# Kernel tuning notes

Hardware: AMD Instinct MI355X
Metric: run time of the kernel (lower is better)

## Reference

```python
import jax, jax.numpy as jnp
import numpy as np

DIM, H, KV, HD = 2048, 32, 8, 64
NREP = H // KV
EPS = 1e-6
NEG = -1e30


def _rope(x, cos, sin):
    # x: [B,S,h,HD], cos/sin: [S,HD//2]
    xr, xi = x[..., 0::2], x[..., 1::2]
    c = cos[None, :, None, :]
    s = sin[None, :, None, :]
    out = jnp.stack([xr * c - xi * s, xr * s + xi * c], axis=-1)
    return out.reshape(x.shape)


def _rmsnorm(x, w):
    xf = x.astype(jnp.float32)
    inv = jax.lax.rsqrt(jnp.mean(xf * xf, axis=-1, keepdims=True) + EPS)
    return (xf * inv * w).astype(x.dtype)


def setup_inputs() -> dict:
    key = jax.random.key(0)
    ks = jax.random.split(key, 9)
    B, S = 1, 2048
    x = jax.random.normal(ks[0], (B, S, DIM), jnp.float32)
    cos = jax.random.uniform(ks[1], (S, HD // 2), jnp.float32)
    sin = jax.random.uniform(ks[2], (S, HD // 2), jnp.float32)
    sc = 1.0 / np.sqrt(DIM)
    wq = jax.random.normal(ks[3], (DIM, DIM), jnp.float32) * sc
    wk = jax.random.normal(ks[4], (KV * HD, DIM), jnp.float32) * sc
    wv = jax.random.normal(ks[5], (KV * HD, DIM), jnp.float32) * sc
    wo = jax.random.normal(ks[6], (DIM, DIM), jnp.float32) * sc
    wg = jax.random.normal(ks[7], (DIM, DIM), jnp.float32) * sc
    qn = jnp.ones((HD,), jnp.float32)
    kn = jnp.ones((HD,), jnp.float32)
    return {"x": x, "cos": cos, "sin": sin, "wq": wq, "wk": wk, "wv": wv,
            "wo": wo, "wg": wg, "qn": qn, "kn": kn}


def reference(x, cos, sin, wq, wk, wv, wo, wg, qn, kn):
    B, S, _ = x.shape
    q = (x @ wq.T).reshape(B, S, H, HD)
    k = (x @ wk.T).reshape(B, S, KV, HD)
    v = (x @ wv.T).reshape(B, S, KV, HD)
    q = _rope(q, cos, sin)
    k = _rope(k, cos, sin)
    q = _rmsnorm(q, qn)
    k = _rmsnorm(k, kn)
    # GQA without materializing repeat_kv: head h = g*NREP + r uses kv head g
    qg = q.reshape(B, S, KV, NREP, HD)
    scale = 1.0 / np.sqrt(HD)
    scores = jnp.einsum('bqgrd,bkgd->bgrqk', qg, k) * scale  # [B,KV,NREP,S,S]
    causal = jnp.tril(jnp.ones((S, S), bool))
    scores = jnp.where(causal, scores, NEG)
    attn = jax.nn.softmax(scores, axis=-1)
    o = jnp.einsum('bgrqk,bkgd->bqgrd', attn, v).reshape(B, S, DIM)
    o = o * jax.nn.sigmoid(x @ wg.T)
    return o @ wo.T
```

## Files before the change

kernel.cpp:

```cpp
#include <hip/hip_runtime.h>
#include <stdint.h>

typedef unsigned short u16;
typedef __bf16 bf16x8 __attribute__((ext_vector_type(8)));
typedef float f32x4 __attribute__((ext_vector_type(4)));

__device__ __forceinline__ float bf2f(u16 u) {
  union { unsigned int i; float f; } v; v.i = ((unsigned int)u) << 16; return v.f;
}
__device__ __forceinline__ u16 f2bf(float f) {
  union { float f; unsigned int i; } v; v.f = f;
  unsigned int r = v.i + 0x7fffu + ((v.i >> 16) & 1u);
  return (u16)(r >> 16);
}
__device__ __forceinline__ u16 f2bf_trunc(float f) {
  union { float f; unsigned int i; } v; v.f = f;
  return (u16)(v.i >> 16);
}
__device__ __forceinline__ void ld16(const void* g, void* l) {
  __builtin_amdgcn_global_load_lds(
      (const __attribute__((address_space(1))) unsigned int*)g,
      (__attribute__((address_space(3))) unsigned int*)l, 16, 0, 0);
}

__global__ __launch_bounds__(256) void k_cast(
    const float* __restrict__ s0, u16* __restrict__ d0,
    const float* __restrict__ s1, u16* __restrict__ d1,
    const float* __restrict__ s2, u16* __restrict__ d2,
    const float* __restrict__ s3, u16* __restrict__ d3,
    const float* __restrict__ s4, u16* __restrict__ d4,
    const float* __restrict__ s5, u16* __restrict__ d5)
{
  int b = blockIdx.x;
  const float* s; u16* d;
  if (b < 4096)       { s = s0; d = d0; }
  else if (b < 8192)  { s = s1; d = d1; b -= 4096; }
  else if (b < 9216)  { s = s2; d = d2; b -= 8192; }
  else if (b < 10240) { s = s3; d = d3; b -= 9216; }
  else if (b < 14336) { s = s4; d = d4; b -= 10240; }
  else                { s = s5; d = d5; b -= 14336; }
  const int i = (b * 256 + threadIdx.x) * 4;
  const float4 v = *(const float4*)(s + i);
  ushort4 o;
  o.x = f2bf(v.x); o.y = f2bf(v.y); o.z = f2bf(v.z); o.w = f2bf(v.w);
  *(ushort4*)(d + i) = o;
}

template <typename OT>
__device__ __forceinline__ void gemm_body(
    const u16* __restrict__ A, int lda,
    const u16* __restrict__ B, int ldb,
    OT* __restrict__ C, int ldc, int K,
    u16* As, u16* Bs)
{
  const int tid = threadIdx.x;
  const int wave = tid >> 6, lane = tid & 63;
  const int wrow = (wave >> 1) * 64, wcol = (wave & 1) * 64;
  const int fr = lane & 15, kg = lane >> 4;
  const int srl = lane >> 3;
  const int scg = (lane & 7) ^ srl;

  f32x4 acc[4][4];
  const f32x4 z = {0.f, 0.f, 0.f, 0.f};
  for (int i = 0; i < 4; i++) for (int j = 0; j < 4; j++) acc[i][j] = z;

  const u16* Ag = A + (size_t)(wave * 8 + srl) * lda + scg * 8;
  const u16* Bg = B + (size_t)(wave * 8 + srl) * ldb + scg * 8;
  u16* Asw = As + wave * 8 * 64;
  u16* Bsw = Bs + wave * 8 * 64;
  const int sxr = fr & 7;

  for (int k0 = 0; k0 < K; k0 += 64) {
    for (int i = 0; i < 4; i++) {
      ld16(Ag + k0 + (size_t)(i * 32) * lda, Asw + i * 32 * 64);
      ld16(Bg + k0 + (size_t)(i * 32) * ldb, Bsw + i * 32 * 64);
    }
    __syncthreads();
    bf16x8 af[4][2], bfr[4][2];
    for (int i = 0; i < 4; i++)
      for (int h = 0; h < 2; h++) {
        af[i][h]  = *(const bf16x8*)&As[(wrow + i * 16 + fr) * 64 + (((h * 4 + kg) ^ sxr)) * 8];
        bfr[i][h] = *(const bf16x8*)&Bs[(wcol + i * 16 + fr) * 64 + (((h * 4 + kg) ^ sxr)) * 8];
      }
    for (int h = 0; h < 2; h++)
      for (int mi = 0; mi < 4; mi++)
        for (int ni = 0; ni < 4; ni++)
          acc[mi][ni] = __builtin_amdgcn_mfma_f32_16x16x32_bf16(af[mi][h], bfr[ni][h], acc[mi][ni], 0, 0, 0);
    __syncthreads();
  }
  const int er = kg * 4, ec = fr;
  for (int mi = 0; mi < 4; mi++)
    for (int ni = 0; ni < 4; ni++)
      for (int r = 0; r < 4; r++) {
        const float v = acc[mi][ni][r];
        OT* p = C + (size_t)(wrow + mi * 16 + er + r) * ldc + wcol + ni * 16 + ec;
        if constexpr (sizeof(OT) == 2) *p = (OT)f2bf(v); else *p = (OT)v;
      }
}

__global__ __launch_bounds__(256) void k_gemm_qkvg(
    const u16* __restrict__ x, const u16* __restrict__ wq, const u16* __restrict__ wk,
    const u16* __restrict__ wv, const u16* __restrict__ wg, u16* __restrict__ out)
{
  __shared__ __align__(16) u16 As[128 * 64];
  __shared__ __align__(16) u16 Bs[128 * 64];
  const int m0 = blockIdx.x * 128;
  const int c0 = blockIdx.y * 128;
  const u16* B; int br;
  if (c0 < 2048)      { B = wq; br = c0; }
  else if (c0 < 2560) { B = wk; br = c0 - 2048; }
  else if (c0 < 3072) { B = wv; br = c0 - 2560; }
  else                { B = wg; br = c0 - 3072; }
  gemm_body<u16>(x + (size_t)m0 * 2048, 2048, B + (size_t)br * 2048, 2048,
                 out + (size_t)m0 * 5120 + c0, 5120, 2048, As, Bs);
}

__global__ __launch_bounds__(256) void k_gemm_out(
    const u16* __restrict__ a, const u16* __restrict__ wo, float* __restrict__ out)
{
  __shared__ __align__(16) u16 As[128 * 64];
  __shared__ __align__(16) u16 Bs[128 * 64];
  const int m0 = blockIdx.x * 128;
  const int c0 = blockIdx.y * 128;
  gemm_body<float>(a + (size_t)m0 * 2048, 2048, wo + (size_t)c0 * 2048, 2048,
                   out + (size_t)m0 * 2048 + c0, 2048, 2048, As, Bs);
}

__global__ __launch_bounds__(256) void k_prep(
    u16* __restrict__ qkvg, const float* __restrict__ cosp, const float* __restrict__ sinp,
    const float* __restrict__ qn, const float* __restrict__ kn, u16* __restrict__ vt)
{
  __shared__ u16 Ls[64 * 72];
  if (blockIdx.x < 10240) {
    const int wid = (blockIdx.x * 256 + threadIdx.x) >> 6;
    const int lane = threadIdx.x & 63;
    const int s = wid / 20, hp = wid - s * 20;
    const int h = hp * 2 + (lane >> 5);
    const int j = lane & 31;
    u16* base; const float* wn;
    if (h < 32) { base = qkvg + (size_t)s * 5120 + h * 64;                wn = qn; }
    else        { base = qkvg + (size_t)s * 5120 + 2048 + (h - 32) * 64; wn = kn; }
    const unsigned int u = *(const unsigned int*)(base + 2 * j);
    const float xr = bf2f((u16)(u & 0xffffu)), xi = bf2f((u16)(u >> 16));
    const float c = cosp[s * 32 + j], sn = sinp[s * 32 + j];
    const float o0 = xr * c - xi * sn;
    const float o1 = xr * sn + xi * c;
    float ss = o0 * o0 + o1 * o1;
    for (int m = 1; m <= 16; m <<= 1) ss += __shfl_xor(ss, m, 64);
    const float inv = rsqrtf(ss * (1.0f / 64.0f) + 1e-6f);
    const u16 r0 = f2bf(o0 * inv * wn[2 * j]);
    const u16 r1 = f2bf(o1 * inv * wn[2 * j + 1]);
    *(unsigned int*)(base + 2 * j) = (unsigned int)r0 | ((unsigned int)r1 << 16);
  } else {
    const int bb = blockIdx.x - 10240;
    const int s0 = (bb & 31) * 64, g0 = (bb >> 5) * 64;
    const int tid = threadIdx.x;
    const int lr = tid >> 4, lc = (tid & 15) * 4;
    for (int p = 0; p < 4; p++) {
      const int r = p * 16 + lr;
      *(ushort4*)&Ls[r * 72 + lc] = *(const ushort4*)&qkvg[(size_t)(s0 + r) * 5120 + 2560 + g0 + lc];
    }
    __syncthreads();
    for (int p = 0; p < 4; p++) {
      const int r = p * 16 + lr;
      ushort4 o;
      o.x = Ls[(lc + 0) * 72 + r];
      o.y = Ls[(lc + 1) * 72 + r];
      o.z = Ls[(lc + 2) * 72 + r];
      o.w = Ls[(lc + 3) * 72 + r];
      *(ushort4*)&vt[(size_t)(g0 + r) * 2048 + s0 + lc] = o;
    }
  }
}

__global__ __launch_bounds__(256) void k_attn_part(
    const u16* __restrict__ qkvg, const u16* __restrict__ vt,
    u16* __restrict__ part, float* __restrict__ ml)
{
  __shared__ __align__(16) u16 Ks[128 * 64];
  __shared__ __align__(16) u16 Vs[64 * 128];
  __shared__ __align__(16) u16 Ps[64 * 132];
  const int c = blockIdx.x, h = blockIdx.y, g = h >> 2;
  int qt, ci;
  if (c < 8)       { qt = c;                 ci = 0; }
  else if (c < 24) { qt = 8 + ((c - 8) >> 1);  ci = (c - 8) & 1; }
  else if (c < 48) { qt = 16 + (c - 24) / 3;   ci = (c - 24) % 3; }
  else             { qt = 24 + ((c - 48) >> 2); ci = (c - 48) & 3; }
  const int kb0 = ci * 512;
  const int kend = min(kb0 + 512, (qt + 1) * 64);
  const int q0 = qt * 64;
  const int tid = threadIdx.x, wave = tid >> 6, lane = tid & 63;
  const int fr = lane & 15, kg = lane >> 4, fq = kg * 8;
  const int sx = fr & 7;

  {
    const u16* Qg = qkvg + (size_t)(q0 + wave * 16 + (lane >> 3)) * 5120 + h * 64 + (lane & 7) * 8;
    ld16(Qg, Ks + wave * 1024);
    ld16(Qg + (size_t)8 * 5120, Ks + wave * 1024 + 512);
  }
  __syncthreads();
  const bf16x8 aq0 = *(const bf16x8*)&Ks[(wave * 16 + fr) * 64 + fq];
  const bf16x8 aq1 = *(const bf16x8*)&Ks[(wave * 16 + fr) * 64 + 32 + fq];
  __syncthreads();

  f32x4 o[4];
  const f32x4 z = {0.f, 0.f, 0.f, 0.f};
  for (int i = 0; i < 4; i++) o[i] = z;
  float lsum[4] = {0.f, 0.f, 0.f, 0.f};
  const int qrow = q0 + wave * 16 + kg * 4;

  const int krl = wave * 8 + (lane >> 3);
  const int kcg = (lane & 7) ^ (krl & 7);
  const int vrl = wave * 4 + kg;
  const int vcg = fr ^ (vrl & 7);

  for (int kb = kb0; kb < kend; kb += 128) {
    {
      const u16* Kg = qkvg + (size_t)(kb + krl) * 5120 + 2048 + g * 64 + kcg * 8;
      for (int i = 0; i < 4; i++)
        ld16(Kg + (size_t)(i * 32) * 5120, Ks + (i * 32 + wave * 8) * 64);
    }
    {
      const u16* Vg = vt + (size_t)(g * 64 + vrl) * 2048 + kb + vcg * 8;
      for (int i = 0; i < 4; i++)
        ld16(Vg + (size_t)(i * 16) * 2048, Vs + (i * 16 + wave * 4) * 128);
    }
    __syncthreads();

    f32x4 sc[8];
    for (int i = 0; i < 8; i++) sc[i] = z;
    for (int ni = 0; ni < 8; ni++) {
      const bf16x8 bk0 = *(const bf16x8*)&Ks[(ni * 16 + fr) * 64 + (kg ^ sx) * 8];
      const bf16x8 bk1 = *(const bf16x8*)&Ks[(ni * 16 + fr) * 64 + ((kg + 4) ^ sx) * 8];
      sc[ni] = __builtin_amdgcn_mfma_f32_16x16x32_bf16(aq0, bk0, sc[ni], 0, 0, 0);
      sc[ni] = __builtin_amdgcn_mfma_f32_16x16x32_bf16(aq1, bk1, sc[ni], 0, 0, 0);
    }

    for (int r = 0; r < 4; r++) {
      float ls = 0.f;
      for (int ni = 0; ni < 8; ni++) {
        const int key = kb + ni * 16 + fr;
        float p = __expf(fmaf(sc[ni][r], 0.125f, -8.0f));
        p = (key <= qrow + r) ? p : 0.f;
        ls += p;
        Ps[(wave * 16 + kg * 4 + r) * 132 + ni * 16 + fr] = f2bf_trunc(p);
      }
      lsum[r] += ls;
    }

    for (int k0 = 0; k0 < 128; k0 += 32) {
      const bf16x8 ap = *(const bf16x8*)&Ps[(wave * 16 + fr) * 132 + k0 + fq];
      for (int ni = 0; ni < 4; ni++) {
        const bf16x8 bv = *(const bf16x8*)&Vs[(ni * 16 + fr) * 128 + (((k0 >> 3) + kg) ^ sx) * 8];
        o[ni] = __builtin_amdgcn_mfma_f32_16x16x32_bf16(ap, bv, o[ni], 0, 0, 0);
      }
    }
    __syncthreads();
  }

  const int pbase = (h * 80 + c) * 4096;
  for (int r = 0; r < 4; r++) {
    float L = lsum[r];
    for (int m = 1; m <= 8; m <<= 1) L += __shfl_xor(L, m, 64);
    const int rl = wave * 16 + kg * 4 + r;
    for (int ni = 0; ni < 4; ni++)
      part[pbase + rl * 64 + ni * 16 + fr] = f2bf(o[ni][r]);
    if (fr == 0) ml[(h * 80 + c) * 64 + rl] = L;
  }
}

__global__ __launch_bounds__(256) void k_attn_comb(
    const u16* __restrict__ part, const float* __restrict__ ml,
    const u16* __restrict__ qkvg, u16* __restrict__ aout)
{
  const int qt = blockIdx.x, h = blockIdx.y;
  const int w = threadIdx.x >> 6, lane = threadIdx.x & 63;
  int cb, nch;
  if (qt < 8)       { cb = qt;               nch = 1; }
  else if (qt < 16) { cb = 8 + 2 * (qt - 8);  nch = 2; }
  else if (qt < 24) { cb = 24 + 3 * (qt - 16); nch = 3; }
  else              { cb = 48 + 4 * (qt - 24); nch = 4; }
  for (int r = 0; r < 16; r++) {
    const int rl = w * 16 + r;
    const int row = qt * 64 + rl;
    float L = 0.f, o = 0.f;
    for (int cc = 0; cc < nch; cc++) {
      L += ml[(h * 80 + cb + cc) * 64 + rl];
      o += bf2f(part[(h * 80 + cb + cc) * 4096 + rl * 64 + lane]);
    }
    const float gv = bf2f(qkvg[(size_t)row * 5120 + 3072 + h * 64 + lane]);
    const float sig = 1.0f / (1.0f + __expf(-gv));
    aout[(size_t)row * 2048 + h * 64 + lane] = f2bf(o / L * sig);
  }
}

extern "C" void kernel_launch(void* const* d_in, const int* in_sizes, int n_in,
                              void* d_out, int out_size, void* d_ws, size_t ws_size,
                              hipStream_t stream)
{
  const float* x  = (const float*)d_in[0];
  const float* cs = (const float*)d_in[1];
  const float* sn = (const float*)d_in[2];
  const float* wq = (const float*)d_in[3];
  const float* wk = (const float*)d_in[4];
  const float* wv = (const float*)d_in[5];
  const float* wo = (const float*)d_in[6];
  const float* wg = (const float*)d_in[7];
  const float* qn = (const float*)d_in[8];
  const float* kn = (const float*)d_in[9];
  float* out = (float*)d_out;

  u16* xb   = (u16*)d_ws;
  u16* wqb  = xb  + (size_t)4194304;
  u16* wkb  = wqb + (size_t)4194304;
  u16* wvb  = wkb + (size_t)1048576;
  u16* wgb  = wvb + (size_t)1048576;
  u16* wob  = wgb + (size_t)4194304;
  u16* qkvg = wob + (size_t)4194304;
  u16* vt   = qkvg + (size_t)2048 * 5120;
  u16* aws  = vt   + (size_t)512 * 2048;

  u16*   part = xb;
  float* ml   = (float*)(xb + (size_t)32 * 80 * 4096);

  k_cast<<<dim3(18432), 256, 0, stream>>>(x, xb, wq, wqb, wk, wkb, wv, wvb, wo, wob, wg, wgb);
  k_gemm_qkvg<<<dim3(16, 40), 256, 0, stream>>>(xb, wqb, wkb, wvb, wgb, qkvg);
  k_prep<<<dim3(10240 + 256), 256, 0, stream>>>(qkvg, cs, sn, qn, kn, vt);
  k_attn_part<<<dim3(80, 32), 256, 0, stream>>>(qkvg, vt, part, ml);
  k_attn_comb<<<dim3(32, 32), 256, 0, stream>>>(part, ml, qkvg, aws);
  k_gemm_out<<<dim3(16, 16), 256, 0, stream>>>(aws, wob, out);
}
```

Measured before the change: 295.4 us.

## Double attention query tile to 128 rows per block for K/V reuse

Each attention block now handles 128 query rows as two 64-row sub-blocks that share every K/V tile loaded into LDS, halving the grid and the combine kernel's tile count. The intent is to halve global K/V traffic and per-tile load and sync overhead per query row. It also sets launch bounds to 3 blocks per CU and hoists the K/V pointer arithmetic out of the loop. In exchange each wave holds twice the accumulators, which raises register pressure, and the coarser causal split leaves fewer, more unevenly sized blocks, reducing parallelism.

```diff
diff --git a/kernel.cpp b/kernel.cpp
--- a/kernel.cpp
+++ b/kernel.cpp
@@ -173,7 +173,7 @@
   }
 }
 
-__global__ __launch_bounds__(256) void k_attn_part(
+__global__ __launch_bounds__(256, 3) void k_attn_part(
     const u16* __restrict__ qkvg, const u16* __restrict__ vt,
     u16* __restrict__ part, float* __restrict__ ml)
 {
@@ -182,91 +182,95 @@
   __shared__ __align__(16) u16 Ps[64 * 132];
   const int c = blockIdx.x, h = blockIdx.y, g = h >> 2;
   int qt, ci;
-  if (c < 8)       { qt = c;                 ci = 0; }
-  else if (c < 24) { qt = 8 + ((c - 8) >> 1);  ci = (c - 8) & 1; }
-  else if (c < 48) { qt = 16 + (c - 24) / 3;   ci = (c - 24) % 3; }
-  else             { qt = 24 + ((c - 48) >> 2); ci = (c - 48) & 3; }
+  if (c < 4)       { qt = c;                  ci = 0; }
+  else if (c < 12) { qt = 4 + ((c - 4) >> 1);   ci = (c - 4) & 1; }
+  else if (c < 24) { qt = 8 + (c - 12) / 3;     ci = (c - 12) % 3; }
+  else             { qt = 12 + ((c - 24) >> 2); ci = (c - 24) & 3; }
   const int kb0 = ci * 512;
-  const int kend = min(kb0 + 512, (qt + 1) * 64);
-  const int q0 = qt * 64;
+  const int kend = min(kb0 + 512, (qt + 1) * 128);
+  const int q0 = qt * 128;
   const int tid = threadIdx.x, wave = tid >> 6, lane = tid & 63;
   const int fr = lane & 15, kg = lane >> 4, fq = kg * 8;
   const int sx = fr & 7;
 
   {
-    const u16* Qg = qkvg + (size_t)(q0 + wave * 16 + (lane >> 3)) * 5120 + h * 64 + (lane & 7) * 8;
-    ld16(Qg, Ks + wave * 1024);
-    ld16(Qg + (size_t)8 * 5120, Ks + wave * 1024 + 512);
+    const u16* Qg = qkvg + (size_t)(q0 + wave * 32 + (lane >> 3)) * 5120 + h * 64 + (lane & 7) * 8;
+    for (int i = 0; i < 4; i++)
+      ld16(Qg + (size_t)(i * 8) * 5120, Ks + (wave * 32 + i * 8) * 64);
   }
   __syncthreads();
-  const bf16x8 aq0 = *(const bf16x8*)&Ks[(wave * 16 + fr) * 64 + fq];
-  const bf16x8 aq1 = *(const bf16x8*)&Ks[(wave * 16 + fr) * 64 + 32 + fq];
+  bf16x8 aq[2][2];
+  for (int rb = 0; rb < 2; rb++) {
+    aq[rb][0] = *(const bf16x8*)&Ks[(rb * 64 + wave * 16 + fr) * 64 + fq];
+    aq[rb][1] = *(const bf16x8*)&Ks[(rb * 64 + wave * 16 + fr) * 64 + 32 + fq];
+  }
   __syncthreads();
 
-  f32x4 o[4];
+  f32x4 o[2][4];
   const f32x4 z = {0.f, 0.f, 0.f, 0.f};
-  for (int i = 0; i < 4; i++) o[i] = z;
-  float lsum[4] = {0.f, 0.f, 0.f, 0.f};
-  const int qrow = q0 + wave * 16 + kg * 4;
+  for (int rb = 0; rb < 2; rb++) for (int i = 0; i < 4; i++) o[rb][i] = z;
+  float lsum[2][4] = {{0.f,0.f,0.f,0.f},{0.f,0.f,0.f,0.f}};
 
   const int krl = wave * 8 + (lane >> 3);
   const int kcg = (lane & 7) ^ (krl & 7);
   const int vrl = wave * 4 + kg;
   const int vcg = fr ^ (vrl & 7);
+  const u16* Kg = qkvg + (size_t)(kb0 + krl) * 5120 + 2048 + g * 64 + kcg * 8;
+  const u16* Vg = vt + (size_t)(g * 64 + vrl) * 2048 + kb0 + vcg * 8;
 
   for (int kb = kb0; kb < kend; kb += 128) {
-    {
-      const u16* Kg = qkvg + (size_t)(kb + krl) * 5120 + 2048 + g * 64 + kcg * 8;
-      for (int i = 0; i < 4; i++)
-        ld16(Kg + (size_t)(i * 32) * 5120, Ks + (i * 32 + wave * 8) * 64);
-    }
-    {
-      const u16* Vg = vt + (size_t)(g * 64 + vrl) * 2048 + kb + vcg * 8;
-      for (int i = 0; i < 4; i++)
-        ld16(Vg + (size_t)(i * 16) * 2048, Vs + (i * 16 + wave * 4) * 128);
-    }
-    __syncthreads();
-
-    f32x4 sc[8];
-    for (int i = 0; i < 8; i++) sc[i] = z;
-    for (int ni = 0; ni < 8; ni++) {
-      const bf16x8 bk0 = *(const bf16x8*)&Ks[(ni * 16 + fr) * 64 + (kg ^ sx) * 8];
-      const bf16x8 bk1 = *(const bf16x8*)&Ks[(ni * 16 + fr) * 64 + ((kg + 4) ^ sx) * 8];
-      sc[ni] = __builtin_amdgcn_mfma_f32_16x16x32_bf16(aq0, bk0, sc[ni], 0, 0, 0);
-      sc[ni] = __builtin_amdgcn_mfma_f32_16x16x32_bf16(aq1, bk1, sc[ni], 0, 0, 0);
-    }
-
+    for (int i = 0; i < 4; i++)
+      ld16(Kg + (size_t)(i * 32) * 5120, Ks + (i * 32 + wave * 8) * 64);
+    for (int i = 0; i < 4; i++)
+      ld16(Vg + (size_t)(i * 16) * 2048, Vs + (i * 16 + wave * 4) * 128);
+    Kg += (size_t)128 * 5120;
+    Vg += 128;
+    __syncthreads();
+
+    for (int rb = 0; rb < 2; rb++) {
+      f32x4 sc[8];
+      for (int i = 0; i < 8; i++) sc[i] = z;
+      for (int ni = 0; ni < 8; ni++) {
+        const bf16x8 bk0 = *(const bf16x8*)&Ks[(ni * 16 + fr) * 64 + (kg ^ sx) * 8];
+        const bf16x8 bk1 = *(const bf16x8*)&Ks[(ni * 16 + fr) * 64 + ((kg + 4) ^ sx) * 8];
+        sc[ni] = __builtin_amdgcn_mfma_f32_16x16x32_bf16(aq[rb][0], bk0, sc[ni], 0, 0, 0);
+        sc[ni] = __builtin_amdgcn_mfma_f32_16x16x32_bf16(aq[rb][1], bk1, sc[ni], 0, 0, 0);
+      }
+
+      const int qrow = q0 + rb * 64 + wave * 16 + kg * 4;
+      for (int r = 0; r < 4; r++) {
+        float ls = 0.f;
+        for (int ni = 0; ni < 8; ni++) {
+          const int key = kb + ni * 16 + fr;
+          float p = __expf(fmaf(sc[ni][r], 0.125f, -8.0f));
+          p = (key <= qrow + r) ? p : 0.f;
+          ls += p;
+          Ps[(wave * 16 + kg * 4 + r) * 132 + ni * 16 + fr] = f2bf_trunc(p);
+        }
+        lsum[rb][r] += ls;
+      }
+
+      for (int k0 = 0; k0 < 128; k0 += 32) {
+        const bf16x8 ap = *(const bf16x8*)&Ps[(wave * 16 + fr) * 132 + k0 + fq];
+        for (int ni = 0; ni < 4; ni++) {
+          const bf16x8 bv = *(const bf16x8*)&Vs[(ni * 16 + fr) * 128 + (((k0 >> 3) + kg) ^ sx) * 8];
+          o[rb][ni] = __builtin_amdgcn_mfma_f32_16x16x32_bf16(ap, bv, o[rb][ni], 0, 0, 0);
+        }
+      }
+    }
+    __syncthreads();
+  }
+
+  const int pbase = (h * 40 + c) * 8192;
+  for (int rb = 0; rb < 2; rb++)
     for (int r = 0; r < 4; r++) {
-      float ls = 0.f;
-      for (int ni = 0; ni < 8; ni++) {
-        const int key = kb + ni * 16 + fr;
-        float p = __expf(fmaf(sc[ni][r], 0.125f, -8.0f));
-        p = (key <= qrow + r) ? p : 0.f;
-        ls += p;
-        Ps[(wave * 16 + kg * 4 + r) * 132 + ni * 16 + fr] = f2bf_trunc(p);
-      }
-      lsum[r] += ls;
-    }
-
-    for (int k0 = 0; k0 < 128; k0 += 32) {
-      const bf16x8 ap = *(const bf16x8*)&Ps[(wave * 16 + fr) * 132 + k0 + fq];
-      for (int ni = 0; ni < 4; ni++) {
-        const bf16x8 bv = *(const bf16x8*)&Vs[(ni * 16 + fr) * 128 + (((k0 >> 3) + kg) ^ sx) * 8];
-        o[ni] = __builtin_amdgcn_mfma_f32_16x16x32_bf16(ap, bv, o[ni], 0, 0, 0);
-      }
-    }
-    __syncthreads();
-  }
-
-  const int pbase = (h * 80 + c) * 4096;
-  for (int r = 0; r < 4; r++) {
-    float L = lsum[r];
-    for (int m = 1; m <= 8; m <<= 1) L += __shfl_xor(L, m, 64);
-    const int rl = wave * 16 + kg * 4 + r;
-    for (int ni = 0; ni < 4; ni++)
-      part[pbase + rl * 64 + ni * 16 + fr] = f2bf(o[ni][r]);
-    if (fr == 0) ml[(h * 80 + c) * 64 + rl] = L;
-  }
+      float L = lsum[rb][r];
+      for (int m = 1; m <= 8; m <<= 1) L += __shfl_xor(L, m, 64);
+      const int rl = rb * 64 + wave * 16 + kg * 4 + r;
+      for (int ni = 0; ni < 4; ni++)
+        part[pbase + rl * 64 + ni * 16 + fr] = f2bf(o[rb][ni][r]);
+      if (fr == 0) ml[(h * 40 + c) * 128 + rl] = L;
+    }
 }
 
 __global__ __launch_bounds__(256) void k_attn_comb(
@@ -276,17 +280,17 @@
   const int qt = blockIdx.x, h = blockIdx.y;
   const int w = threadIdx.x >> 6, lane = threadIdx.x & 63;
   int cb, nch;
-  if (qt < 8)       { cb = qt;               nch = 1; }
-  else if (qt < 16) { cb = 8 + 2 * (qt - 8);  nch = 2; }
-  else if (qt < 24) { cb = 24 + 3 * (qt - 16); nch = 3; }
-  else              { cb = 48 + 4 * (qt - 24); nch = 4; }
-  for (int r = 0; r < 16; r++) {
-    const int rl = w * 16 + r;
-    const int row = qt * 64 + rl;
+  if (qt < 4)       { cb = qt;                nch = 1; }
+  else if (qt < 8)  { cb = 4 + 2 * (qt - 4);   nch = 2; }
+  else if (qt < 12) { cb = 12 + 3 * (qt - 8);  nch = 3; }
+  else              { cb = 24 + 4 * (qt - 12); nch = 4; }
+  for (int r = 0; r < 32; r++) {
+    const int rl = w * 32 + r;
+    const int row = qt * 128 + rl;
     float L = 0.f, o = 0.f;
     for (int cc = 0; cc < nch; cc++) {
-      L += ml[(h * 80 + cb + cc) * 64 + rl];
-      o += bf2f(part[(h * 80 + cb + cc) * 4096 + rl * 64 + lane]);
+      L += ml[(h * 40 + cb + cc) * 128 + rl];
+      o += bf2f(part[(h * 40 + cb + cc) * 8192 + rl * 64 + lane]);
     }
     const float gv = bf2f(qkvg[(size_t)row * 5120 + 3072 + h * 64 + lane]);
     const float sig = 1.0f / (1.0f + __expf(-gv));
@@ -321,12 +325,12 @@
   u16* aws  = vt   + (size_t)512 * 2048;
 
   u16*   part = xb;
-  float* ml   = (float*)(xb + (size_t)32 * 80 * 4096);
+  float* ml   = (float*)(xb + (size_t)32 * 40 * 8192);
 
   k_cast<<<dim3(18432), 256, 0, stream>>>(x, xb, wq, wqb, wk, wkb, wv, wvb, wo, wob, wg, wgb);
   k_gemm_qkvg<<<dim3(16, 40), 256, 0, stream>>>(xb, wqb, wkb, wvb, wgb, qkvg);
   k_prep<<<dim3(10240 + 256), 256, 0, stream>>>(qkvg, cs, sn, qn, kn, vt);
-  k_attn_part<<<dim3(80, 32), 256, 0, stream>>>(qkvg, vt, part, ml);
-  k_attn_comb<<<dim3(32, 32), 256, 0, stream>>>(part, ml, qkvg, aws);
+  k_attn_part<<<dim3(40, 32), 256, 0, stream>>>(qkvg, vt, part, ml);
+  k_attn_comb<<<dim3(16, 32), 256, 0, stream>>>(part, ml, qkvg, aws);
   k_gemm_out<<<dim3(16, 16), 256, 0, stream>>>(aws, wob, out);
 }
```

Result: slower. 316.1 us (+7.0%).
